# Kernel optimization log

Hardware: AMD Instinct MI355X
Metric: run time of the kernel (lower is better)

Reference implementation:

```python
import jax, jax.numpy as jnp
import numpy as np

N_QUBITS = 10
N_LAYERS = 4
BATCH = 4096


def _apply_1q_batched(state, gate, q):
    # state: [B, 2,2,...,2]; gate: [B, 2, 2] (per-sample angles)
    s = jnp.moveaxis(state, 1 + q, -1)
    s = jnp.einsum('b...i,bji->b...j', s, gate)
    return jnp.moveaxis(s, -1, 1 + q)


def _apply_1q(state, gate, q):
    # gate: [2, 2] shared across batch
    s = jnp.moveaxis(state, 1 + q, -1)
    s = jnp.einsum('b...i,ji->b...j', s, gate)
    return jnp.moveaxis(s, -1, 1 + q)


def _apply_cnot(state, c, t):
    # bring control axis to 1 and target axis to 2, flip target where control==1
    s = jnp.moveaxis(state, (1 + c, 1 + t), (1, 2))
    s = jnp.concatenate([s[:, :1], s[:, 1:, ::-1]], axis=1)
    return jnp.moveaxis(s, (1, 2), (1 + c, 1 + t))


def _ry_rz_gate(theta_y, theta_z):
    # RZ(theta_z) @ RY(theta_y), both scalars -> [2, 2] complex
    hy = theta_y * 0.5
    cy, sy = jnp.cos(hy), jnp.sin(hy)
    ry = jnp.stack([jnp.stack([cy, -sy]), jnp.stack([sy, cy])]).astype(jnp.complex64)
    hz = theta_z * 0.5
    ph = jnp.exp(1j * jnp.stack([-hz, hz]).astype(jnp.complex64))  # diag of RZ
    return ph[:, None] * ry


def setup_inputs() -> dict:
    key = jax.random.key(0)
    kx, kp = jax.random.split(key)
    x = jax.random.uniform(kx, (BATCH, N_QUBITS), dtype=jnp.float32,
                           minval=-np.pi, maxval=np.pi)
    params = 0.5 * jax.random.normal(kp, (N_LAYERS, 2 * N_QUBITS), dtype=jnp.float32)
    return {"x": x, "params": params}


def reference(x, params):
    B, n = x.shape
    L = params.shape[0]
    dim = 2 ** n
    # |0...0> for every sample
    state = jnp.zeros((B, dim), jnp.complex64).at[:, 0].set(1.0)
    state = state.reshape((B,) + (2,) * n)

    # data encoding: RY(x[b, q]) on qubit q, per-sample angles
    half = x * 0.5
    c, s = jnp.cos(half), jnp.sin(half)  # [B, n]
    for q in range(n):
        g = jnp.stack([jnp.stack([c[:, q], -s[:, q]], -1),
                       jnp.stack([s[:, q], c[:, q]], -1)], -2).astype(jnp.complex64)  # [B,2,2]
        state = _apply_1q_batched(state, g, q)

    # variational layers: RY then RZ (fused) per qubit, then CNOT ring
    for l in range(L):
        for q in range(n):
            state = _apply_1q(state, _ry_rz_gate(params[l, q], params[l, n + q]), q)
        for q in range(n):
            state = _apply_cnot(state, q, (q + 1) % n)

    # <Z_q> = sum over basis states of |amp|^2 * (+1 if bit_q==0 else -1)
    probs = jnp.abs(state.reshape(B, dim)) ** 2  # float32 [B, 2^n]
    idx = jnp.arange(dim)
    bits = (idx[None, :] >> (n - 1 - jnp.arange(n))[:, None]) & 1  # [n, 2^n]
    signs = (1.0 - 2.0 * bits).astype(probs.dtype)
    return jnp.einsum('bs,qs->bq', probs, signs)  # [B, n]
```

## Files before the change

### kernel.cpp

```cpp
#include <hip/hip_runtime.h>

#define NQ 10

#if __has_builtin(__builtin_amdgcn_permlane16_swap)
#define HAVE_PLSWAP 1
#endif

template<int M>
__device__ __forceinline__ float lx(float v) {
    if constexpr (M == 1)
        return __int_as_float(__builtin_amdgcn_mov_dpp(__float_as_int(v), 0xB1, 0xF, 0xF, true));
    else if constexpr (M == 2)
        return __int_as_float(__builtin_amdgcn_mov_dpp(__float_as_int(v), 0x4E, 0xF, 0xF, true));
    else if constexpr (M == 4) {
        int t = __builtin_amdgcn_mov_dpp(__float_as_int(v), 0x141, 0xF, 0xF, true);
        return __int_as_float(__builtin_amdgcn_mov_dpp(t, 0x1B, 0xF, 0xF, true));
    } else if constexpr (M == 8)
        return __int_as_float(__builtin_amdgcn_mov_dpp(__float_as_int(v), 0x128, 0xF, 0xF, true));
    else if constexpr (M == 16)
        return __int_as_float(__builtin_amdgcn_ds_swizzle(__float_as_int(v), (16 << 10) | 0x1F));
    else
        return __shfl_xor(v, M, 64);
}

template<int M>
__device__ __forceinline__ float2 lx2(float2 v) {
    return make_float2(lx<M>(v.x), lx<M>(v.y));
}

template<int M>
__device__ __forceinline__ void xch(float& a, float& b) {
#ifdef HAVE_PLSWAP
    if constexpr (M == 16) {
        auto r1 = __builtin_amdgcn_permlane16_swap(__float_as_uint(a), __float_as_uint(b), false, false);
        auto r2 = __builtin_amdgcn_permlane16_swap(r1[1], r1[0], false, false);
        a = __uint_as_float(r2[0]);
        b = __uint_as_float(r2[1]);
    } else {
        auto r1 = __builtin_amdgcn_permlane32_swap(__float_as_uint(a), __float_as_uint(b), false, false);
        auto r2 = __builtin_amdgcn_permlane32_swap(r1[1], r1[0], false, false);
        a = __uint_as_float(r2[0]);
        b = __uint_as_float(r2[1]);
    }
#else
    a = lx<M>(a);
    b = lx<M>(b);
#endif
}

__device__ __forceinline__ float2 cmul(float2 a, float2 b) {
    return make_float2(a.x * b.x - a.y * b.y, a.x * b.y + a.y * b.x);
}

__device__ __forceinline__ float2 bperm2(int addr, float2 v) {
    float2 r;
    r.x = __int_as_float(__builtin_amdgcn_ds_bpermute(addr, __float_as_int(v.x)));
    r.y = __int_as_float(__builtin_amdgcn_ds_bpermute(addr, __float_as_int(v.y)));
    return r;
}

template<int M>
__device__ __forceinline__ void ry_lane(float2 st[16], int lane, float c, float s) {
    const float cB = (lane & M) ? s : -s;
#pragma unroll
    for (int r = 0; r < 16; ++r) {
        float2 part = lx2<M>(st[r]);
        st[r].x = c * st[r].x + cB * part.x;
        st[r].y = c * st[r].y + cB * part.y;
    }
}

template<int M>
__device__ __forceinline__ void ry_lane_x(float2 st[16], int lane, float c, float s) {
    const float cB = (lane & M) ? s : -s;
#pragma unroll
    for (int r = 0; r < 16; r += 2) {
        float pax = st[r].x, pay = st[r].y, pbx = st[r + 1].x, pby = st[r + 1].y;
        xch<M>(pax, pbx);
        xch<M>(pay, pby);
        st[r].x     = c * st[r].x     + cB * pax;
        st[r].y     = c * st[r].y     + cB * pay;
        st[r + 1].x = c * st[r + 1].x + cB * pbx;
        st[r + 1].y = c * st[r + 1].y + cB * pby;
    }
}

template<int RB>
__device__ __forceinline__ void ry_reg(float2 st[16], float c, float s) {
#pragma unroll
    for (int r = 0; r < 16; ++r) {
        if (r & RB) continue;
        float2 a0 = st[r], a1 = st[r | RB];
        st[r].x = c * a0.x - s * a1.x;
        st[r].y = c * a0.y - s * a1.y;
        st[r | RB].x = s * a0.x + c * a1.x;
        st[r | RB].y = s * a0.y + c * a1.y;
    }
}

template<int MC, int RB>
__device__ __forceinline__ void cnot_lane_reg(float2 st[16], int lane) {
    const bool sel = (lane & MC) != 0;
#pragma unroll
    for (int r = 0; r < 16; ++r) {
        if (r & RB) continue;
        float2 lo = st[r], hi = st[r | RB];
        st[r]      = sel ? hi : lo;
        st[r | RB] = sel ? lo : hi;
    }
}

template<int RC, int RT>
__device__ __forceinline__ void cnot_reg_reg(float2 st[16]) {
#pragma unroll
    for (int r = 0; r < 16; ++r) {
        if ((r & RC) && !(r & RT)) {
            float2 t = st[r];
            st[r] = st[r | RT];
            st[r | RT] = t;
        }
    }
}

__device__ __forceinline__ void cnot_q9_q0(float2 st[16]) {
#pragma unroll
    for (int i = 0; i < 4; ++i) {
        const int ra = 4 * i + 1, rb = 4 * i + 3;
        xch<32>(st[ra].x, st[rb].x);
        xch<32>(st[ra].y, st[rb].y);
    }
}

__device__ __forceinline__ float wht64(float v, int lane) {
    float t;
    t = lx<1>(v);  v = (lane & 1)  ? (t - v) : (v + t);
    t = lx<2>(v);  v = (lane & 2)  ? (t - v) : (v + t);
    t = lx<4>(v);  v = (lane & 4)  ? (t - v) : (v + t);
    t = lx<8>(v);  v = (lane & 8)  ? (t - v) : (v + t);
    t = lx<16>(v); v = (lane & 16) ? (t - v) : (v + t);
    t = lx<32>(v); v = (lane & 32) ? (t - v) : (v + t);
    return v;
}

__global__ __launch_bounds__(256)
void pqc_kernel(const float* __restrict__ x,
                const float* __restrict__ params,
                float* __restrict__ out, int B) {
    const int lane = threadIdx.x & 63;
    const int wave = threadIdx.x >> 6;
    const int b = blockIdx.x * 4 + wave;
    if (b >= B) return;

    const float* xb = x + (long)b * NQ;
    const float* p0 = params;
    float a0,b0,a1,b1,a2,b2,a3,b3,a4,b4,a5,b5,a6,b6,a7,b7,a8,b8,a9,b9;
    float cz0,sz0,cz1,sz1,cz2,sz2,cz3,sz3,cz4,sz4,cz5,sz5,cz6,sz6,cz7,sz7,cz8,sz8,cz9,sz9;
    __sincosf(0.5f * (xb[0] + p0[0]), &b0, &a0);
    __sincosf(0.5f * (xb[1] + p0[1]), &b1, &a1);
    __sincosf(0.5f * (xb[2] + p0[2]), &b2, &a2);
    __sincosf(0.5f * (xb[3] + p0[3]), &b3, &a3);
    __sincosf(0.5f * (xb[4] + p0[4]), &b4, &a4);
    __sincosf(0.5f * (xb[5] + p0[5]), &b5, &a5);
    __sincosf(0.5f * (xb[6] + p0[6]), &b6, &a6);
    __sincosf(0.5f * (xb[7] + p0[7]), &b7, &a7);
    __sincosf(0.5f * (xb[8] + p0[8]), &b8, &a8);
    __sincosf(0.5f * (xb[9] + p0[9]), &b9, &a9);
    __sincosf(0.5f * p0[10], &sz0, &cz0);
    __sincosf(0.5f * p0[11], &sz1, &cz1);
    __sincosf(0.5f * p0[12], &sz2, &cz2);
    __sincosf(0.5f * p0[13], &sz3, &cz3);
    __sincosf(0.5f * p0[14], &sz4, &cz4);
    __sincosf(0.5f * p0[15], &sz5, &cz5);
    __sincosf(0.5f * p0[16], &sz6, &cz6);
    __sincosf(0.5f * p0[17], &sz7, &cz7);
    __sincosf(0.5f * p0[18], &sz8, &cz8);
    __sincosf(0.5f * p0[19], &sz9, &cz9);

    float R = ((lane & 32) ? b0 : a0) * ((lane & 16) ? b1 : a1)
            * ((lane & 8)  ? b2 : a2) * ((lane & 4)  ? b3 : a3)
            * ((lane & 2)  ? b4 : a4) * ((lane & 1)  ? b5 : a5);
    float2 P = make_float2(cz0, (lane & 32) ? sz0 : -sz0);
    P = cmul(P, make_float2(cz1, (lane & 16) ? sz1 : -sz1));
    P = cmul(P, make_float2(cz2, (lane & 8)  ? sz2 : -sz2));
    P = cmul(P, make_float2(cz3, (lane & 4)  ? sz3 : -sz3));
    P = cmul(P, make_float2(cz4, (lane & 2)  ? sz4 : -sz4));
    P = cmul(P, make_float2(cz5, (lane & 1)  ? sz5 : -sz5));
    float2 laneC = make_float2(R * P.x, R * P.y);

    float2 u6l = make_float2(a6 * cz6, -a6 * sz6), u6h = make_float2(b6 * cz6, b6 * sz6);
    float2 u7l = make_float2(a7 * cz7, -a7 * sz7), u7h = make_float2(b7 * cz7, b7 * sz7);
    float2 u8l = make_float2(a8 * cz8, -a8 * sz8), u8h = make_float2(b8 * cz8, b8 * sz8);
    float2 u9l = make_float2(a9 * cz9, -a9 * sz9), u9h = make_float2(b9 * cz9, b9 * sz9);
    float2 A2[4] = { cmul(u6l, u7l), cmul(u6l, u7h), cmul(u6h, u7l), cmul(u6h, u7h) };
    float2 B2[4] = { cmul(u8l, u9l), cmul(u8l, u9h), cmul(u8h, u9l), cmul(u8h, u9h) };
    float2 LA[4] = { cmul(laneC, A2[0]), cmul(laneC, A2[1]),
                     cmul(laneC, A2[2]), cmul(laneC, A2[3]) };

    float2 st[16];
#pragma unroll
    for (int r = 0; r < 16; ++r) st[r] = cmul(LA[r >> 2], B2[r & 3]);

    {
        const int addr = ((lane ^ (lane >> 1)) & 63) << 2;
#pragma unroll
        for (int r = 0; r < 16; ++r) st[r] = bperm2(addr, st[r]);
        cnot_lane_reg<1, 8>(st, lane);
        cnot_reg_reg<8, 4>(st);
        cnot_reg_reg<4, 2>(st);
        cnot_reg_reg<2, 1>(st);
        cnot_q9_q0(st);
    }

    float c, s;
#pragma unroll
    for (int l = 1; l < 4; ++l) {
        const float* pl = params + l * 2 * NQ;

        __sincosf(0.5f * pl[0], &s, &c); ry_lane_x<32>(st, lane, c, s);
        __sincosf(0.5f * pl[1], &s, &c); ry_lane_x<16>(st, lane, c, s);
        __sincosf(0.5f * pl[2], &s, &c); ry_lane<8>(st, lane, c, s);
        __sincosf(0.5f * pl[3], &s, &c); ry_lane<4>(st, lane, c, s);
        __sincosf(0.5f * pl[4], &s, &c); ry_lane<2>(st, lane, c, s);
        __sincosf(0.5f * pl[5], &s, &c); ry_lane<1>(st, lane, c, s);
        __sincosf(0.5f * pl[6], &s, &c); ry_reg<8>(st, c, s);
        __sincosf(0.5f * pl[7], &s, &c); ry_reg<4>(st, c, s);
        __sincosf(0.5f * pl[8], &s, &c); ry_reg<2>(st, c, s);
        __sincosf(0.5f * pl[9], &s, &c); ry_reg<1>(st, c, s);

        if (l < 3) {
            float sz, cz;
            __sincosf(0.5f * pl[10], &sz, &cz);
            float2 PL = make_float2(cz, (lane & 32) ? sz : -sz);
            __sincosf(0.5f * pl[11], &sz, &cz);
            PL = cmul(PL, make_float2(cz, (lane & 16) ? sz : -sz));
            __sincosf(0.5f * pl[12], &sz, &cz);
            PL = cmul(PL, make_float2(cz, (lane & 8) ? sz : -sz));
            __sincosf(0.5f * pl[13], &sz, &cz);
            PL = cmul(PL, make_float2(cz, (lane & 4) ? sz : -sz));
            __sincosf(0.5f * pl[14], &sz, &cz);
            PL = cmul(PL, make_float2(cz, (lane & 2) ? sz : -sz));
            __sincosf(0.5f * pl[15], &sz, &cz);
            PL = cmul(PL, make_float2(cz, (lane & 1) ? sz : -sz));

            float z6s, z6c, z7s, z7c, z8s, z8c, z9s, z9c;
            __sincosf(0.5f * pl[16], &z6s, &z6c);
            __sincosf(0.5f * pl[17], &z7s, &z7c);
            __sincosf(0.5f * pl[18], &z8s, &z8c);
            __sincosf(0.5f * pl[19], &z9s, &z9c);
            float2 A[4], Bb[4];
#pragma unroll
            for (int k = 0; k < 4; ++k) {
                A[k] = cmul(cmul(make_float2(z6c, (k & 2) ? z6s : -z6s),
                                 make_float2(z7c, (k & 1) ? z7s : -z7s)), PL);
                Bb[k] = cmul(make_float2(z8c, (k & 2) ? z8s : -z8s),
                             make_float2(z9c, (k & 1) ? z9s : -z9s));
            }
#pragma unroll
            for (int r = 0; r < 16; ++r)
                st[r] = cmul(cmul(st[r], A[r >> 2]), Bb[r & 3]);

            const int addr = ((lane ^ (lane >> 1)) & 63) << 2;
#pragma unroll
            for (int r = 0; r < 16; ++r) st[r] = bperm2(addr, st[r]);
            cnot_lane_reg<1, 8>(st, lane);
            cnot_reg_reg<8, 4>(st);
            cnot_reg_reg<4, 2>(st);
            cnot_reg_reg<2, 1>(st);
            cnot_q9_q0(st);
        }
    }

    float lane_sum = 0.f, A3 = 0.f, A32 = 0.f, A321 = 0.f, A3210 = 0.f;
#pragma unroll
    for (int r = 0; r < 16; ++r) {
        float p = st[r].x * st[r].x + st[r].y * st[r].y;
        const int p3 = (r >> 3) & 1;
        const int p32 = p3 ^ ((r >> 2) & 1);
        const int p321 = p32 ^ ((r >> 1) & 1);
        const int p3210 = p321 ^ (r & 1);
        lane_sum += p;
        A3    += p3    ? -p : p;
        A32   += p32   ? -p : p;
        A321  += p321  ? -p : p;
        A3210 += p3210 ? -p : p;
    }
    const float wLS   = wht64(lane_sum, lane);
    const float w3    = wht64(A3, lane);
    const float w32   = wht64(A32, lane);
    const float w321  = wht64(A321, lane);
    const float w3210 = wht64(A3210, lane);

    const long base = (long)b * NQ;
    if (lane == 31) out[base + 0] = w3210;
    if (lane == 48) out[base + 1] = wLS;
    if (lane == 56) out[base + 2] = wLS;
    if (lane == 60) out[base + 3] = wLS;
    if (lane == 62) out[base + 4] = wLS;
    if (lane == 63) {
        out[base + 5] = wLS;
        out[base + 6] = w3;
        out[base + 7] = w32;
        out[base + 8] = w321;
        out[base + 9] = w3210;
    }
}

extern "C" void kernel_launch(void* const* d_in, const int* in_sizes, int n_in,
                              void* d_out, int out_size, void* d_ws, size_t ws_size,
                              hipStream_t stream) {
    const float* x = (const float*)d_in[0];
    const float* params = (const float*)d_in[1];
    float* out = (float*)d_out;
    const int B = in_sizes[0] / NQ;
    const int grid = (B + 3) / 4;
    pqc_kernel<<<grid, 256, 0, stream>>>(x, params, out, B);
}
```

Baseline: 82.81 us.

## Split each sample's statevector across two waves with LDS exchange

```diff
diff --git a/kernel.cpp b/kernel.cpp
--- a/kernel.cpp
+++ b/kernel.cpp
@@ -60,10 +60,10 @@
 }
 
 template<int M>
-__device__ __forceinline__ void ry_lane(float2 st[16], int lane, float c, float s) {
+__device__ __forceinline__ void ry_lane(float2 st[8], int lane, float c, float s) {
     const float cB = (lane & M) ? s : -s;
 #pragma unroll
-    for (int r = 0; r < 16; ++r) {
+    for (int r = 0; r < 8; ++r) {
         float2 part = lx2<M>(st[r]);
         st[r].x = c * st[r].x + cB * part.x;
         st[r].y = c * st[r].y + cB * part.y;
@@ -71,10 +71,10 @@
 }
 
 template<int M>
-__device__ __forceinline__ void ry_lane_x(float2 st[16], int lane, float c, float s) {
+__device__ __forceinline__ void ry_lane_x(float2 st[8], int lane, float c, float s) {
     const float cB = (lane & M) ? s : -s;
 #pragma unroll
-    for (int r = 0; r < 16; r += 2) {
+    for (int r = 0; r < 8; r += 2) {
         float pax = st[r].x, pay = st[r].y, pbx = st[r + 1].x, pby = st[r + 1].y;
         xch<M>(pax, pbx);
         xch<M>(pay, pby);
@@ -86,9 +86,9 @@
 }
 
 template<int RB>
-__device__ __forceinline__ void ry_reg(float2 st[16], float c, float s) {
-#pragma unroll
-    for (int r = 0; r < 16; ++r) {
+__device__ __forceinline__ void ry_reg(float2 st[8], float c, float s) {
+#pragma unroll
+    for (int r = 0; r < 8; ++r) {
         if (r & RB) continue;
         float2 a0 = st[r], a1 = st[r | RB];
         st[r].x = c * a0.x - s * a1.x;
@@ -98,36 +98,19 @@
     }
 }
 
-template<int MC, int RB>
-__device__ __forceinline__ void cnot_lane_reg(float2 st[16], int lane) {
-    const bool sel = (lane & MC) != 0;
-#pragma unroll
-    for (int r = 0; r < 16; ++r) {
-        if (r & RB) continue;
-        float2 lo = st[r], hi = st[r | RB];
-        st[r]      = sel ? hi : lo;
-        st[r | RB] = sel ? lo : hi;
-    }
-}
-
-template<int RC, int RT>
-__device__ __forceinline__ void cnot_reg_reg(float2 st[16]) {
-#pragma unroll
-    for (int r = 0; r < 16; ++r) {
-        if ((r & RC) && !(r & RT)) {
-            float2 t = st[r];
-            st[r] = st[r | RT];
-            st[r | RT] = t;
-        }
-    }
-}
-
-__device__ __forceinline__ void cnot_q9_q0(float2 st[16]) {
-#pragma unroll
-    for (int i = 0; i < 4; ++i) {
-        const int ra = 4 * i + 1, rb = 4 * i + 3;
-        xch<32>(st[ra].x, st[rb].x);
-        xch<32>(st[ra].y, st[rb].y);
+__device__ __forceinline__ void xw_write(const float2 st[8], float* buf, int tid) {
+    float4* row = (float4*)(buf + tid * 16);
+#pragma unroll
+    for (int k = 0; k < 4; ++k)
+        row[k] = make_float4(st[2 * k].x, st[2 * k].y, st[2 * k + 1].x, st[2 * k + 1].y);
+}
+__device__ __forceinline__ void xw_read(float2 p[8], const float* buf, int ptid) {
+    const float4* row = (const float4*)(buf + ptid * 16);
+#pragma unroll
+    for (int k = 0; k < 4; ++k) {
+        float4 v = row[k];
+        p[2 * k]     = make_float2(v.x, v.y);
+        p[2 * k + 1] = make_float2(v.z, v.w);
     }
 }
 
@@ -142,14 +125,16 @@
     return v;
 }
 
-__global__ __launch_bounds__(256)
+__global__ __launch_bounds__(128, 8)
 void pqc_kernel(const float* __restrict__ x,
                 const float* __restrict__ params,
                 float* __restrict__ out, int B) {
-    const int lane = threadIdx.x & 63;
-    const int wave = threadIdx.x >> 6;
-    const int b = blockIdx.x * 4 + wave;
-    if (b >= B) return;
+    const int tid  = threadIdx.x;
+    const int lane = tid & 63;
+    const int wid  = tid >> 6;
+    const int b    = blockIdx.x;
+
+    __shared__ float buf[128 * 16];
 
     const float* xb = x + (long)b * NQ;
     const float* p0 = params;
@@ -187,29 +172,53 @@
     P = cmul(P, make_float2(cz5, (lane & 1)  ? sz5 : -sz5));
     float2 laneC = make_float2(R * P.x, R * P.y);
 
-    float2 u6l = make_float2(a6 * cz6, -a6 * sz6), u6h = make_float2(b6 * cz6, b6 * sz6);
+    float2 u6w = wid ? make_float2(b6 * cz6,  b6 * sz6)
+                     : make_float2(a6 * cz6, -a6 * sz6);
     float2 u7l = make_float2(a7 * cz7, -a7 * sz7), u7h = make_float2(b7 * cz7, b7 * sz7);
     float2 u8l = make_float2(a8 * cz8, -a8 * sz8), u8h = make_float2(b8 * cz8, b8 * sz8);
     float2 u9l = make_float2(a9 * cz9, -a9 * sz9), u9h = make_float2(b9 * cz9, b9 * sz9);
-    float2 A2[4] = { cmul(u6l, u7l), cmul(u6l, u7h), cmul(u6h, u7l), cmul(u6h, u7h) };
-    float2 B2[4] = { cmul(u8l, u9l), cmul(u8l, u9h), cmul(u8h, u9l), cmul(u8h, u9h) };
-    float2 LA[4] = { cmul(laneC, A2[0]), cmul(laneC, A2[1]),
-                     cmul(laneC, A2[2]), cmul(laneC, A2[3]) };
-
-    float2 st[16];
-#pragma unroll
-    for (int r = 0; r < 16; ++r) st[r] = cmul(LA[r >> 2], B2[r & 3]);
-
-    {
+
+    float2 LW = cmul(laneC, u6w);
+    float2 LWA[4] = { cmul(LW, cmul(u7l, u8l)), cmul(LW, cmul(u7l, u8h)),
+                      cmul(LW, cmul(u7h, u8l)), cmul(LW, cmul(u7h, u8h)) };
+    float2 B2[2] = { u9l, u9h };
+
+    float2 st[8];
+#pragma unroll
+    for (int r = 0; r < 8; ++r) st[r] = cmul(LWA[r >> 1], B2[r & 1]);
+
+    auto ring = [&]() {
         const int addr = ((lane ^ (lane >> 1)) & 63) << 2;
 #pragma unroll
-        for (int r = 0; r < 16; ++r) st[r] = bperm2(addr, st[r]);
-        cnot_lane_reg<1, 8>(st, lane);
-        cnot_reg_reg<8, 4>(st);
-        cnot_reg_reg<4, 2>(st);
-        cnot_reg_reg<2, 1>(st);
-        cnot_q9_q0(st);
-    }
+        for (int r = 0; r < 8; ++r) st[r] = bperm2(addr, st[r]);
+        xw_write(st, buf, tid);
+        __syncthreads();
+        {
+            float2 p[8];
+            xw_read(p, buf, tid ^ 64);
+            const bool sel = (lane & 1) != 0;
+#pragma unroll
+            for (int r = 0; r < 8; ++r) st[r] = sel ? p[r] : st[r];
+        }
+        __syncthreads();
+        {
+            const bool sel = wid != 0;
+#pragma unroll
+            for (int r = 0; r < 4; ++r) {
+                float2 lo = st[r], hi = st[r + 4];
+                st[r]     = sel ? hi : lo;
+                st[r + 4] = sel ? lo : hi;
+            }
+        }
+        { float2 t = st[4]; st[4] = st[6]; st[6] = t; }
+        { float2 t = st[5]; st[5] = st[7]; st[7] = t; }
+        { float2 t = st[2]; st[2] = st[3]; st[3] = t; }
+        { float2 t = st[6]; st[6] = st[7]; st[7] = t; }
+        xch<32>(st[1].x, st[3].x); xch<32>(st[1].y, st[3].y);
+        xch<32>(st[5].x, st[7].x); xch<32>(st[5].y, st[7].y);
+    };
+
+    ring();
 
     float c, s;
 #pragma unroll
@@ -222,86 +231,101 @@
         __sincosf(0.5f * pl[3], &s, &c); ry_lane<4>(st, lane, c, s);
         __sincosf(0.5f * pl[4], &s, &c); ry_lane<2>(st, lane, c, s);
         __sincosf(0.5f * pl[5], &s, &c); ry_lane<1>(st, lane, c, s);
-        __sincosf(0.5f * pl[6], &s, &c); ry_reg<8>(st, c, s);
+        {
+            __sincosf(0.5f * pl[6], &s, &c);
+            xw_write(st, buf, tid);
+            __syncthreads();
+            float2 p[8];
+            xw_read(p, buf, tid ^ 64);
+            const float cB = wid ? s : -s;
+#pragma unroll
+            for (int r = 0; r < 8; ++r) {
+                st[r].x = c * st[r].x + cB * p[r].x;
+                st[r].y = c * st[r].y + cB * p[r].y;
+            }
+            __syncthreads();
+        }
         __sincosf(0.5f * pl[7], &s, &c); ry_reg<4>(st, c, s);
         __sincosf(0.5f * pl[8], &s, &c); ry_reg<2>(st, c, s);
         __sincosf(0.5f * pl[9], &s, &c); ry_reg<1>(st, c, s);
 
         if (l < 3) {
-            float sz, cz;
-            __sincosf(0.5f * pl[10], &sz, &cz);
-            float2 PL = make_float2(cz, (lane & 32) ? sz : -sz);
-            __sincosf(0.5f * pl[11], &sz, &cz);
-            PL = cmul(PL, make_float2(cz, (lane & 16) ? sz : -sz));
-            __sincosf(0.5f * pl[12], &sz, &cz);
-            PL = cmul(PL, make_float2(cz, (lane & 8) ? sz : -sz));
-            __sincosf(0.5f * pl[13], &sz, &cz);
-            PL = cmul(PL, make_float2(cz, (lane & 4) ? sz : -sz));
-            __sincosf(0.5f * pl[14], &sz, &cz);
-            PL = cmul(PL, make_float2(cz, (lane & 2) ? sz : -sz));
-            __sincosf(0.5f * pl[15], &sz, &cz);
-            PL = cmul(PL, make_float2(cz, (lane & 1) ? sz : -sz));
-
-            float z6s, z6c, z7s, z7c, z8s, z8c, z9s, z9c;
-            __sincosf(0.5f * pl[16], &z6s, &z6c);
+            float szq, czq;
+            __sincosf(0.5f * pl[10], &szq, &czq);
+            float2 PL = make_float2(czq, (lane & 32) ? szq : -szq);
+            __sincosf(0.5f * pl[11], &szq, &czq);
+            PL = cmul(PL, make_float2(czq, (lane & 16) ? szq : -szq));
+            __sincosf(0.5f * pl[12], &szq, &czq);
+            PL = cmul(PL, make_float2(czq, (lane & 8) ? szq : -szq));
+            __sincosf(0.5f * pl[13], &szq, &czq);
+            PL = cmul(PL, make_float2(czq, (lane & 4) ? szq : -szq));
+            __sincosf(0.5f * pl[14], &szq, &czq);
+            PL = cmul(PL, make_float2(czq, (lane & 2) ? szq : -szq));
+            __sincosf(0.5f * pl[15], &szq, &czq);
+            PL = cmul(PL, make_float2(czq, (lane & 1) ? szq : -szq));
+            __sincosf(0.5f * pl[16], &szq, &czq);
+            PL = cmul(PL, make_float2(czq, wid ? szq : -szq));
+            float z7s, z7c, z8s, z8c, z9s, z9c;
             __sincosf(0.5f * pl[17], &z7s, &z7c);
             __sincosf(0.5f * pl[18], &z8s, &z8c);
             __sincosf(0.5f * pl[19], &z9s, &z9c);
-            float2 A[4], Bb[4];
-#pragma unroll
-            for (int k = 0; k < 4; ++k) {
-                A[k] = cmul(cmul(make_float2(z6c, (k & 2) ? z6s : -z6s),
-                                 make_float2(z7c, (k & 1) ? z7s : -z7s)), PL);
-                Bb[k] = cmul(make_float2(z8c, (k & 2) ? z8s : -z8s),
-                             make_float2(z9c, (k & 1) ? z9s : -z9s));
-            }
-#pragma unroll
-            for (int r = 0; r < 16; ++r)
-                st[r] = cmul(cmul(st[r], A[r >> 2]), Bb[r & 3]);
-
-            const int addr = ((lane ^ (lane >> 1)) & 63) << 2;
-#pragma unroll
-            for (int r = 0; r < 16; ++r) st[r] = bperm2(addr, st[r]);
-            cnot_lane_reg<1, 8>(st, lane);
-            cnot_reg_reg<8, 4>(st);
-            cnot_reg_reg<4, 2>(st);
-            cnot_reg_reg<2, 1>(st);
-            cnot_q9_q0(st);
-        }
-    }
-
-    float lane_sum = 0.f, A3 = 0.f, A32 = 0.f, A321 = 0.f, A3210 = 0.f;
-#pragma unroll
-    for (int r = 0; r < 16; ++r) {
+            float2 PLA[4], zB[2];
+#pragma unroll
+            for (int k = 0; k < 4; ++k)
+                PLA[k] = cmul(PL, cmul(make_float2(z7c, (k & 2) ? z7s : -z7s),
+                                       make_float2(z8c, (k & 1) ? z8s : -z8s)));
+            zB[0] = make_float2(z9c, -z9s);
+            zB[1] = make_float2(z9c,  z9s);
+#pragma unroll
+            for (int r = 0; r < 8; ++r)
+                st[r] = cmul(cmul(st[r], PLA[r >> 1]), zB[r & 1]);
+
+            ring();
+        }
+    }
+
+    float S = 0.f, S4 = 0.f, S6 = 0.f, S7 = 0.f;
+#pragma unroll
+    for (int r = 0; r < 8; ++r) {
         float p = st[r].x * st[r].x + st[r].y * st[r].y;
-        const int p3 = (r >> 3) & 1;
-        const int p32 = p3 ^ ((r >> 2) & 1);
-        const int p321 = p32 ^ ((r >> 1) & 1);
-        const int p3210 = p321 ^ (r & 1);
-        lane_sum += p;
-        A3    += p3    ? -p : p;
-        A32   += p32   ? -p : p;
-        A321  += p321  ? -p : p;
-        A3210 += p3210 ? -p : p;
-    }
-    const float wLS   = wht64(lane_sum, lane);
-    const float w3    = wht64(A3, lane);
-    const float w32   = wht64(A32, lane);
-    const float w321  = wht64(A321, lane);
-    const float w3210 = wht64(A3210, lane);
-
-    const long base = (long)b * NQ;
-    if (lane == 31) out[base + 0] = w3210;
-    if (lane == 48) out[base + 1] = wLS;
-    if (lane == 56) out[base + 2] = wLS;
-    if (lane == 60) out[base + 3] = wLS;
-    if (lane == 62) out[base + 4] = wLS;
-    if (lane == 63) {
-        out[base + 5] = wLS;
-        out[base + 6] = w3;
-        out[base + 7] = w32;
-        out[base + 8] = w321;
-        out[base + 9] = w3210;
+        const int p2 = (r >> 2) & 1;
+        const int p21 = p2 ^ ((r >> 1) & 1);
+        const int p210 = p21 ^ (r & 1);
+        S  += p;
+        S4 += p2   ? -p : p;
+        S6 += p21  ? -p : p;
+        S7 += p210 ? -p : p;
+    }
+    const float ws = wid ? -1.f : 1.f;
+    float A = S, Bv = ws * S, C = ws * S4, D = ws * S6, E = ws * S7;
+
+    {
+        float* row = buf + tid * 16;
+        row[0] = A; row[1] = Bv; row[2] = C; row[3] = D; row[4] = E;
+        __syncthreads();
+        const float* pr = buf + (tid ^ 64) * 16;
+        A += pr[0]; Bv += pr[1]; C += pr[2]; D += pr[3]; E += pr[4];
+    }
+
+    if (wid == 0) {
+        const float wA = wht64(A, lane);
+        const float wB = wht64(Bv, lane);
+        const float wC = wht64(C, lane);
+        const float wD = wht64(D, lane);
+        const float wE = wht64(E, lane);
+        const long base = (long)b * NQ;
+        if (lane == 31) out[base + 0] = wE;
+        if (lane == 48) out[base + 1] = wA;
+        if (lane == 56) out[base + 2] = wA;
+        if (lane == 60) out[base + 3] = wA;
+        if (lane == 62) out[base + 4] = wA;
+        if (lane == 63) {
+            out[base + 5] = wA;
+            out[base + 6] = wB;
+            out[base + 7] = wC;
+            out[base + 8] = wD;
+            out[base + 9] = wE;
+        }
     }
 }
 
@@ -312,6 +336,5 @@
     const float* params = (const float*)d_in[1];
     float* out = (float*)d_out;
     const int B = in_sizes[0] / NQ;
-    const int grid = (B + 3) / 4;
-    pqc_kernel<<<grid, 256, 0, stream>>>(x, params, out, B);
-}
+    pqc_kernel<<<B, 128, 0, stream>>>(x, params, out, B);
+}
```

After: 97.12 us. 17.3% more time.
